# Performance work log

Measured on AMD Instinct MI355X. Metric: run time of the kernel, lower is better.

## Reference

```python
import jax, jax.numpy as jnp
import numpy as np

DIM = 1024
HEADS = 16
DIM_HEAD = 64
INNER = HEADS * DIM_HEAD  # 1024
SCALE = DIM_HEAD ** -0.5


def setup_inputs() -> dict:
    key = jax.random.key(0)
    k1, k2, k3, k4 = jax.random.split(key, 4)
    B, N = 4, 2048
    x = jax.random.normal(k1, (B, N, DIM), dtype=jnp.float32)
    # Linear weights stored as [in, out] so y = x @ W (+ b)
    W_qkv = jax.random.normal(k2, (DIM, 3 * INNER), dtype=jnp.float32) * (DIM ** -0.5)
    W_out = jax.random.normal(k3, (INNER, DIM), dtype=jnp.float32) * (INNER ** -0.5)
    b_out = jax.random.normal(k4, (DIM,), dtype=jnp.float32) * 0.01
    return {"x": x, "W_qkv": W_qkv, "W_out": W_out, "b_out": b_out}


def reference(x, W_qkv, W_out, b_out):
    B, N, _ = x.shape
    qkv = x @ W_qkv  # [B, N, 3*INNER]
    q, k, v = jnp.split(qkv, 3, axis=-1)
    # [B, N, H, Dh] -> [B, H, N, Dh]
    reshape = lambda t: t.reshape(B, N, HEADS, DIM_HEAD).transpose(0, 2, 1, 3)
    q, k, v = reshape(q), reshape(k), reshape(v)
    dots = jnp.einsum("bhqd,bhkd->bhqk", q, k) * SCALE  # [B,H,N,N]
    attn = jax.nn.softmax(dots, axis=-1)
    out = jnp.einsum("bhqk,bhkd->bhqd", attn, v)  # [B,H,N,Dh]
    out = out.transpose(0, 2, 1, 3).reshape(B, N, INNER)
    return out @ W_out + b_out
```

## Files before the change

kernel.cpp:

```cpp
#include <hip/hip_runtime.h>


typedef _Float16 half8 __attribute__((ext_vector_type(8)));
typedef __fp16 fp16v2 __attribute__((ext_vector_type(2)));
typedef float floatx4 __attribute__((ext_vector_type(4)));
typedef unsigned short u16;

struct __align__(8) U16x4 { u16 x, y, z, w; };

__device__ __forceinline__ u16 f2h(float f) {
  union { _Float16 h; u16 u; } cv;
  cv.h = (_Float16)f;
  return cv.u;
}

__device__ __forceinline__ void g2l16(const void* g, void* l) {
  __builtin_amdgcn_global_load_lds(
      (const __attribute__((address_space(1))) void*)g,
      (__attribute__((address_space(3))) void*)l, 16, 0, 0);
}

__device__ __forceinline__ int swz(int c) { return (c & 3) ^ ((c >> 3) & 3); }

__global__ __launch_bounds__(256) void cast_f32_f16(const float* __restrict__ in,
                                                    u16* __restrict__ out) {
  long long base = ((long long)blockIdx.x * 256 + threadIdx.x) * 8;
  float4 a = *(const float4*)(in + base);
  float4 b = *(const float4*)(in + base + 4);
  U16x4 u0 = {f2h(a.x), f2h(a.y), f2h(a.z), f2h(a.w)};
  U16x4 u1 = {f2h(b.x), f2h(b.y), f2h(b.z), f2h(b.w)};
  *(U16x4*)(out + base) = u0;
  *(U16x4*)(out + base + 4) = u1;
}

__global__ __launch_bounds__(256) void transpose_cast(const float* __restrict__ in,
                                                      u16* __restrict__ out,
                                                      int K, int N) {
  __shared__ u16 ls[64][72];
  const int nTK = K >> 6;
  const int tk = blockIdx.x % nTK;
  const int tn = blockIdx.x / nTK;
  const int tid = threadIdx.x;
#pragma unroll
  for (int i = 0; i < 4; ++i) {
    int idx = i * 256 + tid;
    int r = idx >> 4, c4 = (idx & 15) * 4;
    float4 v = *(const float4*)(in + (long long)(tk * 64 + r) * N + tn * 64 + c4);
    ls[r][c4 + 0] = f2h(v.x);
    ls[r][c4 + 1] = f2h(v.y);
    ls[r][c4 + 2] = f2h(v.z);
    ls[r][c4 + 3] = f2h(v.w);
  }
  __syncthreads();
#pragma unroll
  for (int i = 0; i < 4; ++i) {
    int idx = i * 256 + tid;
    int nr = idx >> 4, kc4 = (idx & 15) * 4;
    U16x4 u = {ls[kc4 + 0][nr], ls[kc4 + 1][nr], ls[kc4 + 2][nr], ls[kc4 + 3][nr]};
    *(U16x4*)(out + (long long)(tn * 64 + nr) * K + tk * 64 + kc4) = u;
  }
}

template <int EPI>
__global__ __launch_bounds__(256) void gemm_f16(const u16* __restrict__ A,
                                                const u16* __restrict__ Bt,
                                                u16* __restrict__ O0,
                                                u16* __restrict__ O1,
                                                u16* __restrict__ O2,
                                                float* __restrict__ Of,
                                                const float* __restrict__ bias) {
  __shared__ __attribute__((aligned(16))) u16 lsA[128 * 32];
  __shared__ __attribute__((aligned(16))) u16 lsB[128 * 32];
  const int tid = threadIdx.x;
  const int lane = tid & 63, wave = tid >> 6;
  const int l15 = lane & 15, quad = lane >> 4;
  const int sw = (l15 >> 1) & 3;
  const int qsw8 = (quad ^ sw) * 8;
  const int wm = (wave >> 1) * 64, wn = (wave & 1) * 64;
  const int bm = blockIdx.x & 63;
  const int bn = blockIdx.x >> 6;

  const int c0 = tid, c1 = 256 + tid;
  const u16* ga0 = A + (long long)(bm * 128 + (c0 >> 2)) * 1024 + swz(c0) * 8;
  const u16* ga1 = A + (long long)(bm * 128 + (c1 >> 2)) * 1024 + swz(c1) * 8;
  const u16* gb0 = Bt + (long long)(bn * 128 + (c0 >> 2)) * 1024 + swz(c0) * 8;
  const u16* gb1 = Bt + (long long)(bn * 128 + (c1 >> 2)) * 1024 + swz(c1) * 8;
  u16* la0 = lsA + (wave * 64) * 8;
  u16* la1 = lsA + (256 + wave * 64) * 8;
  u16* lb0 = lsB + (wave * 64) * 8;
  u16* lb1 = lsB + (256 + wave * 64) * 8;

  floatx4 acc[4][4] = {};

  for (int kt = 0; kt < 32; ++kt) {
    const int ko = kt * 32;
    g2l16(ga0 + ko, la0);
    g2l16(ga1 + ko, la1);
    g2l16(gb0 + ko, lb0);
    g2l16(gb1 + ko, lb1);
    __syncthreads();
    half8 af[4], bf[4];
#pragma unroll
    for (int mt = 0; mt < 4; ++mt)
      af[mt] = *(const half8*)(lsA + (wm + mt * 16 + l15) * 32 + qsw8);
#pragma unroll
    for (int nt = 0; nt < 4; ++nt)
      bf[nt] = *(const half8*)(lsB + (wn + nt * 16 + l15) * 32 + qsw8);
#pragma unroll
    for (int mt = 0; mt < 4; ++mt)
#pragma unroll
      for (int nt = 0; nt < 4; ++nt)
        acc[mt][nt] = __builtin_amdgcn_mfma_f32_16x16x32_f16(af[mt], bf[nt], acc[mt][nt], 0, 0, 0);
    __syncthreads();
  }

  if (EPI == 0) {
    const float slq = 0.125f * 1.44269504088896f;
#pragma unroll
    for (int mt = 0; mt < 4; ++mt) {
      int gm = bm * 128 + wm + mt * 16 + quad * 4;
      int b = gm >> 11, n0 = gm & 2047;
#pragma unroll
      for (int nt = 0; nt < 4; ++nt) {
        int gc = bn * 128 + wn + nt * 16 + l15;
        int t = gc >> 10, hd = gc & 1023, h = hd >> 6, d = hd & 63;
        long long bh = (long long)(b * 16 + h);
        if (t == 2) {
          U16x4 u = {f2h(acc[mt][nt][0]), f2h(acc[mt][nt][1]),
                     f2h(acc[mt][nt][2]), f2h(acc[mt][nt][3])};
          *(U16x4*)(O2 + (bh * 64 + d) * 2048 + n0) = u;
        } else {
          float s = (t == 0) ? slq : 1.0f;
          u16* dst = (t == 0 ? O0 : O1) + (bh * 2048 + n0) * 64 + d;
#pragma unroll
          for (int r = 0; r < 4; ++r) dst[r * 64] = f2h(acc[mt][nt][r] * s);
        }
      }
    }
  } else {
#pragma unroll
    for (int mt = 0; mt < 4; ++mt) {
      int gm = bm * 128 + wm + mt * 16 + quad * 4;
#pragma unroll
      for (int nt = 0; nt < 4; ++nt) {
        int gc = bn * 128 + wn + nt * 16 + l15;
        float bv = bias[gc];
#pragma unroll
        for (int r = 0; r < 4; ++r)
          Of[(long long)(gm + r) * 1024 + gc] = acc[mt][nt][r] + bv;
      }
    }
  }
}

__global__ __launch_bounds__(256, 4) void attn_flash(const u16* __restrict__ Qh,
                                                     const u16* __restrict__ Kh,
                                                     const u16* __restrict__ Vt,
                                                     u16* __restrict__ Oh) {
  __shared__ __attribute__((aligned(16))) u16 lsK[2 * 128 * 32];
  __shared__ __attribute__((aligned(16))) u16 lsV[4 * 64 * 32];
  __shared__ __attribute__((aligned(16))) u16 lsP[4 * 32 * 32];
  const int tid = threadIdx.x;
  const int lane = tid & 63, wave = tid >> 6;
  const int l15 = lane & 15, quad = lane >> 4;
  const int sw = (l15 >> 1) & 3;
  const int qsw8 = (quad ^ sw) * 8;
  const int bh = blockIdx.x & 63, qt = blockIdx.x >> 6;
  const u16* Qb = Qh + ((long long)bh * 2048 + qt * 128) * 64;
  const u16* Kb = Kh + (long long)bh * 2048 * 64;
  const u16* Vb = Vt + (long long)bh * 64 * 2048;
  u16* lsPw = lsP + wave * 1024;

#pragma unroll
  for (int i = 0; i < 4; ++i) {
    int c = i * 256 + tid;
    g2l16(Qb + ((c >> 2) & 127) * 64 + (c >> 9) * 32 + swz(c) * 8,
          lsK + (i * 256 + wave * 64) * 8);
  }
  __syncthreads();
  half8 qb[2][2];
#pragma unroll
  for (int qt2 = 0; qt2 < 2; ++qt2)
#pragma unroll
    for (int ks = 0; ks < 2; ++ks)
      qb[qt2][ks] = *(const half8*)(lsK + ks * 4096 + (wave * 32 + qt2 * 16 + l15) * 32 + qsw8);
  __syncthreads();

#pragma unroll
  for (int i = 0; i < 4; ++i) {
    int c = i * 256 + tid;
    g2l16(Kb + ((c >> 2) & 127) * 64 + (c >> 9) * 32 + swz(c) * 8,
          lsK + (i * 256 + wave * 64) * 8);
    g2l16(Vb + ((c >> 2) & 63) * 2048 + (c >> 8) * 32 + swz(c) * 8,
          lsV + (i * 256 + wave * 64) * 8);
  }
  __syncthreads();

  half8 onesf;
#pragma unroll
  for (int j = 0; j < 8; ++j) onesf[j] = (_Float16)1.0f;

  floatx4 oacc[2][4] = {};
  floatx4 osum[2] = {};

  for (int kt = 0; kt < 16; ++kt) {
#pragma unroll
    for (int ks4 = 0; ks4 < 4; ++ks4) {
      floatx4 sacc[2][2] = {};
#pragma unroll
      for (int ks = 0; ks < 2; ++ks) {
#pragma unroll
        for (int h = 0; h < 2; ++h) {
          half8 kf = *(const half8*)(lsK + ks * 4096 + ((ks4 * 2 + h) * 16 + l15) * 32 + qsw8);
          sacc[h][0] = __builtin_amdgcn_mfma_f32_16x16x32_f16(kf, qb[0][ks], sacc[h][0], 0, 0, 0);
          sacc[h][1] = __builtin_amdgcn_mfma_f32_16x16x32_f16(kf, qb[1][ks], sacc[h][1], 0, 0, 0);
        }
      }
#pragma unroll
      for (int h = 0; h < 2; ++h) {
#pragma unroll
        for (int qt2 = 0; qt2 < 2; ++qt2) {
          float p0 = __builtin_amdgcn_exp2f(sacc[h][qt2][0]);
          float p1 = __builtin_amdgcn_exp2f(sacc[h][qt2][1]);
          float p2 = __builtin_amdgcn_exp2f(sacc[h][qt2][2]);
          float p3 = __builtin_amdgcn_exp2f(sacc[h][qt2][3]);
          union { fp16v2 h2; unsigned u; } lo, hi;
          lo.h2 = __builtin_amdgcn_cvt_pkrtz(p0, p1);
          hi.h2 = __builtin_amdgcn_cvt_pkrtz(p2, p3);
          uint2 pk = {lo.u, hi.u};
          *(uint2*)(lsPw + (qt2 * 16 + l15) * 32 +
                    (((2 * h + (quad >> 1)) ^ sw) * 8) + (quad & 1) * 4) = pk;
        }
      }
      half8 pa0 = *(const half8*)(lsPw + l15 * 32 + qsw8);
      half8 pa1 = *(const half8*)(lsPw + (16 + l15) * 32 + qsw8);
#pragma unroll
      for (int dt = 0; dt < 4; ++dt) {
        half8 vb = *(const half8*)(lsV + ks4 * 2048 + (dt * 16 + l15) * 32 + qsw8);
        oacc[0][dt] = __builtin_amdgcn_mfma_f32_16x16x32_f16(pa0, vb, oacc[0][dt], 0, 0, 0);
        oacc[1][dt] = __builtin_amdgcn_mfma_f32_16x16x32_f16(pa1, vb, oacc[1][dt], 0, 0, 0);
      }
      osum[0] = __builtin_amdgcn_mfma_f32_16x16x32_f16(pa0, onesf, osum[0], 0, 0, 0);
      osum[1] = __builtin_amdgcn_mfma_f32_16x16x32_f16(pa1, onesf, osum[1], 0, 0, 0);
    }
    if (kt < 15) {
      __syncthreads();
#pragma unroll
      for (int i = 0; i < 4; ++i) {
        int c = i * 256 + tid;
        g2l16(Kb + (kt + 1) * 8192 + ((c >> 2) & 127) * 64 + (c >> 9) * 32 + swz(c) * 8,
              lsK + (i * 256 + wave * 64) * 8);
        g2l16(Vb + ((c >> 2) & 63) * 2048 + (kt + 1) * 128 + (c >> 8) * 32 + swz(c) * 8,
              lsV + (i * 256 + wave * 64) * 8);
      }
      __syncthreads();
    }
  }

  const int b = bh >> 4, h = bh & 15;
#pragma unroll
  for (int qt2 = 0; qt2 < 2; ++qt2) {
#pragma unroll
    for (int r = 0; r < 4; ++r) {
      float inv = 1.0f / osum[qt2][r];
      int qrow = qt * 128 + wave * 32 + qt2 * 16 + quad * 4 + r;
      long long rowbase = ((long long)b * 2048 + qrow) * 1024 + h * 64;
#pragma unroll
      for (int dt = 0; dt < 4; ++dt)
        Oh[rowbase + dt * 16 + l15] = f2h(oacc[qt2][dt][r] * inv);
    }
  }
}

extern "C" void kernel_launch(void* const* d_in, const int* in_sizes, int n_in,
                              void* d_out, int out_size, void* d_ws, size_t ws_size,
                              hipStream_t stream) {
  const float* x = (const float*)d_in[0];
  const float* Wqkv = (const float*)d_in[1];
  const float* Wout = (const float*)d_in[2];
  const float* bout = (const float*)d_in[3];
  float* out = (float*)d_out;

  char* ws = (char*)d_ws;
  u16* Xh = (u16*)(ws);
  u16* Wqkvt = (u16*)(ws + (16ll << 20));
  u16* Woutt = (u16*)(ws + (22ll << 20));
  u16* Qh = (u16*)(ws + (24ll << 20));
  u16* Kh = (u16*)(ws + (40ll << 20));
  u16* Vt = (u16*)(ws + (56ll << 20));
  u16* Oh = (u16*)(ws + (72ll << 20));

  cast_f32_f16<<<4096, 256, 0, stream>>>(x, Xh);
  transpose_cast<<<16 * 48, 256, 0, stream>>>(Wqkv, Wqkvt, 1024, 3072);
  transpose_cast<<<16 * 16, 256, 0, stream>>>(Wout, Woutt, 1024, 1024);
  gemm_f16<0><<<64 * 24, 256, 0, stream>>>(Xh, Wqkvt, Qh, Kh, Vt, nullptr, nullptr);
  attn_flash<<<1024, 256, 0, stream>>>(Qh, Kh, Vt, Oh);
  gemm_f16<1><<<64 * 8, 256, 0, stream>>>(Oh, Woutt, nullptr, nullptr, nullptr, out, bout);
}
```

Baseline: 271.5 us.

## Double-buffer K/V tiles in flash attention and deepen GEMM K-tile

The attention kernel now streams K and V in 64-key tiles through two LDS buffers. The next tile's async global-to-LDS load is issued right after a single barrier, so it overlaps with the current tile's compute and the second barrier per iteration goes away. The QKV/output GEMM doubles its K-step to 64 with an 8-way XOR swizzle and adds an occupancy hint, which halves the number of barrier-separated load rounds. The trade-offs are twice as many attention loop iterations, and the risk that the compiler inserts full vmcnt waits that serialize the prefetch anyway.

After: 264.3 us. 1.03x faster.

```diff
diff --git a/kernel.cpp b/kernel.cpp
--- a/kernel.cpp
+++ b/kernel.cpp
@@ -21,6 +21,7 @@
 }
 
 __device__ __forceinline__ int swz(int c) { return (c & 3) ^ ((c >> 3) & 3); }
+__device__ __forceinline__ int swz8(int s) { return (s & 7) ^ ((s >> 3) & 7); }
 
 __global__ __launch_bounds__(256) void cast_f32_f16(const float* __restrict__ in,
                                                     u16* __restrict__ out) {
@@ -62,55 +63,61 @@
 }
 
 template <int EPI>
-__global__ __launch_bounds__(256) void gemm_f16(const u16* __restrict__ A,
-                                                const u16* __restrict__ Bt,
-                                                u16* __restrict__ O0,
-                                                u16* __restrict__ O1,
-                                                u16* __restrict__ O2,
-                                                float* __restrict__ Of,
-                                                const float* __restrict__ bias) {
-  __shared__ __attribute__((aligned(16))) u16 lsA[128 * 32];
-  __shared__ __attribute__((aligned(16))) u16 lsB[128 * 32];
+__global__ __launch_bounds__(256, 4) void gemm_f16(const u16* __restrict__ A,
+                                                   const u16* __restrict__ Bt,
+                                                   u16* __restrict__ O0,
+                                                   u16* __restrict__ O1,
+                                                   u16* __restrict__ O2,
+                                                   float* __restrict__ Of,
+                                                   const float* __restrict__ bias) {
+  __shared__ __attribute__((aligned(16))) u16 lsA[128 * 64];
+  __shared__ __attribute__((aligned(16))) u16 lsB[128 * 64];
   const int tid = threadIdx.x;
   const int lane = tid & 63, wave = tid >> 6;
   const int l15 = lane & 15, quad = lane >> 4;
-  const int sw = (l15 >> 1) & 3;
-  const int qsw8 = (quad ^ sw) * 8;
+  const int w7 = l15 & 7;
+  const int offk0 = ((quad) ^ w7) * 8;
+  const int offk1 = ((4 + quad) ^ w7) * 8;
   const int wm = (wave >> 1) * 64, wn = (wave & 1) * 64;
   const int bm = blockIdx.x & 63;
   const int bn = blockIdx.x >> 6;
 
-  const int c0 = tid, c1 = 256 + tid;
-  const u16* ga0 = A + (long long)(bm * 128 + (c0 >> 2)) * 1024 + swz(c0) * 8;
-  const u16* ga1 = A + (long long)(bm * 128 + (c1 >> 2)) * 1024 + swz(c1) * 8;
-  const u16* gb0 = Bt + (long long)(bn * 128 + (c0 >> 2)) * 1024 + swz(c0) * 8;
-  const u16* gb1 = Bt + (long long)(bn * 128 + (c1 >> 2)) * 1024 + swz(c1) * 8;
-  u16* la0 = lsA + (wave * 64) * 8;
-  u16* la1 = lsA + (256 + wave * 64) * 8;
-  u16* lb0 = lsB + (wave * 64) * 8;
-  u16* lb1 = lsB + (256 + wave * 64) * 8;
+  const u16* ga[4];
+  const u16* gb[4];
+#pragma unroll
+  for (int i = 0; i < 4; ++i) {
+    int s = i * 256 + tid;
+    ga[i] = A + (long long)(bm * 128 + (s >> 3)) * 1024 + swz8(s) * 8;
+    gb[i] = Bt + (long long)(bn * 128 + (s >> 3)) * 1024 + swz8(s) * 8;
+  }
 
   floatx4 acc[4][4] = {};
 
-  for (int kt = 0; kt < 32; ++kt) {
-    const int ko = kt * 32;
-    g2l16(ga0 + ko, la0);
-    g2l16(ga1 + ko, la1);
-    g2l16(gb0 + ko, lb0);
-    g2l16(gb1 + ko, lb1);
+  for (int kt = 0; kt < 16; ++kt) {
+    const int ko = kt * 64;
+#pragma unroll
+    for (int i = 0; i < 4; ++i)
+      g2l16(ga[i] + ko, lsA + (i * 256 + wave * 64) * 8);
+#pragma unroll
+    for (int i = 0; i < 4; ++i)
+      g2l16(gb[i] + ko, lsB + (i * 256 + wave * 64) * 8);
     __syncthreads();
-    half8 af[4], bf[4];
-#pragma unroll
-    for (int mt = 0; mt < 4; ++mt)
-      af[mt] = *(const half8*)(lsA + (wm + mt * 16 + l15) * 32 + qsw8);
-#pragma unroll
-    for (int nt = 0; nt < 4; ++nt)
-      bf[nt] = *(const half8*)(lsB + (wn + nt * 16 + l15) * 32 + qsw8);
-#pragma unroll
-    for (int mt = 0; mt < 4; ++mt)
+#pragma unroll
+    for (int ks = 0; ks < 2; ++ks) {
+      const int off = ks ? offk1 : offk0;
+      half8 af[4], bf[4];
+#pragma unroll
+      for (int mt = 0; mt < 4; ++mt)
+        af[mt] = *(const half8*)(lsA + (wm + mt * 16 + l15) * 64 + off);
 #pragma unroll
       for (int nt = 0; nt < 4; ++nt)
-        acc[mt][nt] = __builtin_amdgcn_mfma_f32_16x16x32_f16(af[mt], bf[nt], acc[mt][nt], 0, 0, 0);
+        bf[nt] = *(const half8*)(lsB + (wn + nt * 16 + l15) * 64 + off);
+#pragma unroll
+      for (int mt = 0; mt < 4; ++mt)
+#pragma unroll
+        for (int nt = 0; nt < 4; ++nt)
+          acc[mt][nt] = __builtin_amdgcn_mfma_f32_16x16x32_f16(af[mt], bf[nt], acc[mt][nt], 0, 0, 0);
+    }
     __syncthreads();
   }
 
@@ -157,8 +164,8 @@
                                                      const u16* __restrict__ Kh,
                                                      const u16* __restrict__ Vt,
                                                      u16* __restrict__ Oh) {
-  __shared__ __attribute__((aligned(16))) u16 lsK[2 * 128 * 32];
-  __shared__ __attribute__((aligned(16))) u16 lsV[4 * 64 * 32];
+  __shared__ __attribute__((aligned(16))) u16 lsK[2 * 2 * 64 * 32];
+  __shared__ __attribute__((aligned(16))) u16 lsV[2 * 2 * 64 * 32];
   __shared__ __attribute__((aligned(16))) u16 lsP[4 * 32 * 32];
   const int tid = threadIdx.x;
   const int lane = tid & 63, wave = tid >> 6;
@@ -187,14 +194,13 @@
   __syncthreads();
 
 #pragma unroll
-  for (int i = 0; i < 4; ++i) {
+  for (int i = 0; i < 2; ++i) {
     int c = i * 256 + tid;
-    g2l16(Kb + ((c >> 2) & 127) * 64 + (c >> 9) * 32 + swz(c) * 8,
+    g2l16(Kb + ((c >> 2) & 63) * 64 + (c >> 8) * 32 + swz(c) * 8,
           lsK + (i * 256 + wave * 64) * 8);
     g2l16(Vb + ((c >> 2) & 63) * 2048 + (c >> 8) * 32 + swz(c) * 8,
           lsV + (i * 256 + wave * 64) * 8);
   }
-  __syncthreads();
 
   half8 onesf;
 #pragma unroll
@@ -203,15 +209,31 @@
   floatx4 oacc[2][4] = {};
   floatx4 osum[2] = {};
 
-  for (int kt = 0; kt < 16; ++kt) {
-#pragma unroll
-    for (int ks4 = 0; ks4 < 4; ++ks4) {
+  for (int kt = 0; kt < 32; ++kt) {
+    const int cur = kt & 1;
+    const u16* bufK = lsK + cur * 4096;
+    const u16* bufV = lsV + cur * 4096;
+    __syncthreads();
+    if (kt < 31) {
+      u16* nK = lsK + (1 - cur) * 4096;
+      u16* nV = lsV + (1 - cur) * 4096;
+#pragma unroll
+      for (int i = 0; i < 2; ++i) {
+        int c = i * 256 + tid;
+        g2l16(Kb + (kt + 1) * 4096 + ((c >> 2) & 63) * 64 + (c >> 8) * 32 + swz(c) * 8,
+              nK + (i * 256 + wave * 64) * 8);
+        g2l16(Vb + ((c >> 2) & 63) * 2048 + (kt + 1) * 64 + (c >> 8) * 32 + swz(c) * 8,
+              nV + (i * 256 + wave * 64) * 8);
+      }
+    }
+#pragma unroll
+    for (int ks4 = 0; ks4 < 2; ++ks4) {
       floatx4 sacc[2][2] = {};
 #pragma unroll
       for (int ks = 0; ks < 2; ++ks) {
 #pragma unroll
         for (int h = 0; h < 2; ++h) {
-          half8 kf = *(const half8*)(lsK + ks * 4096 + ((ks4 * 2 + h) * 16 + l15) * 32 + qsw8);
+          half8 kf = *(const half8*)(bufK + ks * 2048 + ((ks4 * 2 + h) * 16 + l15) * 32 + qsw8);
           sacc[h][0] = __builtin_amdgcn_mfma_f32_16x16x32_f16(kf, qb[0][ks], sacc[h][0], 0, 0, 0);
           sacc[h][1] = __builtin_amdgcn_mfma_f32_16x16x32_f16(kf, qb[1][ks], sacc[h][1], 0, 0, 0);
         }
@@ -236,24 +258,12 @@
       half8 pa1 = *(const half8*)(lsPw + (16 + l15) * 32 + qsw8);
 #pragma unroll
       for (int dt = 0; dt < 4; ++dt) {
-        half8 vb = *(const half8*)(lsV + ks4 * 2048 + (dt * 16 + l15) * 32 + qsw8);
+        half8 vb = *(const half8*)(bufV + ks4 * 2048 + (dt * 16 + l15) * 32 + qsw8);
         oacc[0][dt] = __builtin_amdgcn_mfma_f32_16x16x32_f16(pa0, vb, oacc[0][dt], 0, 0, 0);
         oacc[1][dt] = __builtin_amdgcn_mfma_f32_16x16x32_f16(pa1, vb, oacc[1][dt], 0, 0, 0);
       }
       osum[0] = __builtin_amdgcn_mfma_f32_16x16x32_f16(pa0, onesf, osum[0], 0, 0, 0);
       osum[1] = __builtin_amdgcn_mfma_f32_16x16x32_f16(pa1, onesf, osum[1], 0, 0, 0);
-    }
-    if (kt < 15) {
-      __syncthreads();
-#pragma unroll
-      for (int i = 0; i < 4; ++i) {
-        int c = i * 256 + tid;
-        g2l16(Kb + (kt + 1) * 8192 + ((c >> 2) & 127) * 64 + (c >> 9) * 32 + swz(c) * 8,
-              lsK + (i * 256 + wave * 64) * 8);
-        g2l16(Vb + ((c >> 2) & 63) * 2048 + (kt + 1) * 128 + (c >> 8) * 32 + swz(c) * 8,
-              lsV + (i * 256 + wave * 64) * 8);
-      }
-      __syncthreads();
     }
   }
 
```
